# Kernel tuning notes

Measured on AMD Instinct MI355X. Metric: run time of the kernel, lower is better.

Reference implementation:

```python
import jax, jax.numpy as jnp
import numpy as np
from jax import lax

B, NR, NT, M, NUM_ITER = 16384, 64, 32, 4, 64


def setup_inputs() -> dict:
    key = jax.random.key(0)
    k1, k2, k3 = jax.random.split(key, 3)
    yt = jax.random.normal(k1, (B, NR), dtype=jnp.float32)
    # scale channel to keep the 64-step unrolled descent numerically stable
    Ht = 0.1 * jax.random.normal(k2, (B, NR, NT), dtype=jnp.float32)
    sigmat0 = 0.5 + 0.5 * jax.random.uniform(k3, (B,), dtype=jnp.float32)
    m = jnp.array([-3.0, -1.0, 1.0, 3.0], dtype=jnp.float32)          # 4-PAM constellation
    alpha = jnp.full((M,), 0.25, dtype=jnp.float32)                    # uniform prior
    taui = jnp.ones((NUM_ITER + 1,), dtype=jnp.float32)                # taui0 = 1
    delta = jnp.full((NUM_ITER,), 0.1, dtype=jnp.float32)              # delta0 = 0.1
    return {"yt": yt, "Ht": Ht, "sigmat0": sigmat0, "m": m, "alpha": alpha,
            "taui": taui, "delta": delta}


def reference(yt, Ht, sigmat0, m, alpha, taui, delta):
    # Precompute as in CMDNet.call
    HH = jnp.einsum('bri,brj->bij', Ht, Ht)          # [B, Nt, Nt] = H^T H
    yH = jnp.einsum('br,brj->bj', yt, Ht)            # [B, Nt]     = y^T H
    Bsz, _, Nt = Ht.shape
    Mc = m.shape[0]
    n_iter = delta.shape[0]

    G0 = jnp.zeros((Bsz, Nt, Mc), dtype=Ht.dtype)
    sig2 = (sigmat0 ** 2)[:, None, None]             # [B,1,1]
    log_alpha = jnp.log(alpha)                       # [M]
    taui_abs = jnp.abs(taui)                         # [num_iter+1]
    # first layer uses scale 1 in the softmax (first_iter=True), but taui_abs in grad_x
    ft_scale = taui_abs[:n_iter].at[0].set(1.0)

    def step(G, inp):
        scale, ta, d = inp
        ft = jax.nn.softmax((log_alpha + G) * scale, axis=-1)   # [B,Nt,M]
        xt = jnp.sum(ft * m, axis=-1)                           # [B,Nt] soft symbol
        xHH = jnp.einsum('bi,bij->bj', xt, HH)                  # [B,Nt]
        grad_x = ta * (ft * m - ft * xt[..., None])             # [B,Nt,M]
        grad_L = sig2 * (1.0 - jnp.exp(-G)) + grad_x * (xHH - yH)[..., None]
        return G - d * grad_L, None

    G, _ = lax.scan(step, G0, (ft_scale, taui_abs[:n_iter], delta))

    # last layer (last_iter=True): softmax + soft symbol only, no update
    ft = jax.nn.softmax((log_alpha + G) * taui_abs[n_iter], axis=-1)
    xt = jnp.sum(ft * m, axis=-1)
    return ft, xt
```

## Files before the change

### kernel.cpp

```cpp
#include <hip/hip_runtime.h>


#define NRr 64
#define NTt 32
#define NITER 64
#define B_TOTAL 16384

using f16x8  = __attribute__((ext_vector_type(8))) _Float16;
using f32x16 = __attribute__((ext_vector_type(16))) float;

__global__ __launch_bounds__(256) void cmdnet_kernel(
    const float* __restrict__ yt,
    const float* __restrict__ Ht,
    const float* __restrict__ sig0,
    const float* __restrict__ mm,
    const float* __restrict__ alpha,
    const float* __restrict__ taui,
    const float* __restrict__ delta,
    float* __restrict__ out)
{
    __shared__ float xts[4][2][32];

    const int tid = threadIdx.x;
    const int w   = tid >> 6;
    const int l   = tid & 63;
    const int j   = l & 31;
    const int hi  = l >> 5;
    const int b0  = (blockIdx.x * 4 + w) * 2;

    f32x16 accA = {}, accB = {};
    float  ypA = 0.f, ypB = 0.f;
#pragma unroll
    for (int bb = 0; bb < 2; ++bb) {
        const int b = b0 + bb;
        const float* hp = Ht + (size_t)b * NRr * NTt + j;
        const float* yp = yt + (size_t)b * NRr;
        f32x16 acc = {};
        float  ypart = 0.f;
#pragma unroll
        for (int kc = 0; kc < 4; ++kc) {
            const int kb = kc * 16 + hi * 8;
            float h[8];
#pragma unroll
            for (int e = 0; e < 8; ++e) h[e] = hp[(size_t)(kb + e) * NTt];
            const float4 ya = *(const float4*)(yp + kb);
            const float4 yb = *(const float4*)(yp + kb + 4);
            ypart += h[0]*ya.x + h[1]*ya.y + h[2]*ya.z + h[3]*ya.w
                   + h[4]*yb.x + h[5]*yb.y + h[6]*yb.z + h[7]*yb.w;
            f16x8 fa;
#pragma unroll
            for (int e = 0; e < 8; ++e) fa[e] = (_Float16)h[e];
            acc = __builtin_amdgcn_mfma_f32_32x32x16_f16(fa, fa, acc, 0, 0, 0);
        }
        if (bb == 0) { accA = acc; ypA = ypart; }
        else         { accB = acc; ypB = ypart; }
    }

    float hh[32];
#pragma unroll
    for (int r = 0; r < 16; ++r) {
        const float own = hi ? accB[r] : accA[r];
        const float snd = hi ? accA[r] : accB[r];
        const float oth = __shfl_xor(snd, 32, 64);
        const int g = r >> 2, k = r & 3;
        hh[8*g + k]     = hi ? oth : own;
        hh[8*g + 4 + k] = hi ? own : oth;
    }
    const float yA = ypA + __shfl_xor(ypA, 32, 64);
    const float yB = ypB + __shfl_xor(ypB, 32, 64);
    const float yH = hi ? yB : yA;

    const int   bmy  = b0 + hi;
    const float sgv  = sig0[bmy];
    const float sig2 = sgv * sgv;

    const float4 mv = *(const float4*)mm;
    const float4 av = *(const float4*)alpha;
    const float m0 = mv.x, m1 = mv.y, m2 = mv.z, m3 = mv.w;
    const float la0 = __logf(av.x), la1 = __logf(av.y),
                la2 = __logf(av.z), la3 = __logf(av.w);

    float G0 = 0.f, G1 = 0.f, G2 = 0.f, G3 = 0.f;

    for (int it = 0; it < NITER; ++it) {
        const float ta = fabsf(taui[it]);
        const float sc = (it == 0) ? 1.0f : ta;
        const float d  = delta[it];

        const float s0 = (la0 + G0) * sc, s1 = (la1 + G1) * sc;
        const float s2 = (la2 + G2) * sc, s3 = (la3 + G3) * sc;
        const float mx = fmaxf(fmaxf(s0, s1), fmaxf(s2, s3));
        const float e0 = __expf(s0 - mx), e1 = __expf(s1 - mx);
        const float e2 = __expf(s2 - mx), e3 = __expf(s3 - mx);
        const float Z  = (e0 + e1) + (e2 + e3);
        const float R  = __builtin_amdgcn_rcpf(Z);
        const float ft0 = e0 * R, ft1 = e1 * R, ft2 = e2 * R, ft3 = e3 * R;
        const float xt  = (ft0*m0 + ft1*m1) + (ft2*m2 + ft3*m3);

        xts[w][hi][j] = xt;
        asm volatile("" ::: "memory");
        float acc = 0.f;
        const float4* xv = (const float4*)&xts[w][hi][0];
#pragma unroll
        for (int q = 0; q < 8; ++q) {
            const float4 x4 = xv[q];
            acc += hh[4*q+0]*x4.x + hh[4*q+1]*x4.y
                 + hh[4*q+2]*x4.z + hh[4*q+3]*x4.w;
        }
        asm volatile("" ::: "memory");

        const float qd  = acc - yH;
        const float tqd = ta * qd * d;
        const float ds2 = d * sig2;
        G0 -= ds2 * (1.f - __expf(-G0)) + tqd * (ft0 * (m0 - xt));
        G1 -= ds2 * (1.f - __expf(-G1)) + tqd * (ft1 * (m1 - xt));
        G2 -= ds2 * (1.f - __expf(-G2)) + tqd * (ft2 * (m2 - xt));
        G3 -= ds2 * (1.f - __expf(-G3)) + tqd * (ft3 * (m3 - xt));
    }

    {
        const float ta = fabsf(taui[NITER]);
        const float s0 = (la0 + G0) * ta, s1 = (la1 + G1) * ta;
        const float s2 = (la2 + G2) * ta, s3 = (la3 + G3) * ta;
        const float mx = fmaxf(fmaxf(s0, s1), fmaxf(s2, s3));
        const float e0 = __expf(s0 - mx), e1 = __expf(s1 - mx);
        const float e2 = __expf(s2 - mx), e3 = __expf(s3 - mx);
        const float Z  = (e0 + e1) + (e2 + e3);
        const float R  = __builtin_amdgcn_rcpf(Z);
        const float ft0 = e0 * R, ft1 = e1 * R, ft2 = e2 * R, ft3 = e3 * R;
        const float xt  = (ft0*m0 + ft1*m1) + (ft2*m2 + ft3*m3);

        float4 f4; f4.x = ft0; f4.y = ft1; f4.z = ft2; f4.w = ft3;
        *(float4*)(out + ((size_t)bmy * NTt + j) * 4) = f4;
        out[(size_t)B_TOTAL * NTt * 4 + (size_t)bmy * NTt + j] = xt;
    }
}

extern "C" void kernel_launch(void* const* d_in, const int* in_sizes, int n_in,
                              void* d_out, int out_size, void* d_ws, size_t ws_size,
                              hipStream_t stream) {
    const float* yt    = (const float*)d_in[0];
    const float* Ht    = (const float*)d_in[1];
    const float* sig0  = (const float*)d_in[2];
    const float* mm    = (const float*)d_in[3];
    const float* alpha = (const float*)d_in[4];
    const float* taui  = (const float*)d_in[5];
    const float* delta = (const float*)d_in[6];
    float* out = (float*)d_out;

    const int blocks = B_TOTAL / 8;
    cmdnet_kernel<<<blocks, 256, 0, stream>>>(yt, Ht, sig0, mm, alpha, taui,
                                              delta, out);
}
```

Baseline: 115.3 us.

## Pack Gram matrix and soft symbols to fp16 and use dot2 in iteration loop

Stores the per-thread row of H^T H as packed fp16 pairs and writes soft symbols to shared memory in fp16. The mat-vec then runs on v_dot2 instructions with two accumulators, halving LDS reads and register use for hh. The change also swaps exp for exp2 with pre-scaled log2e constants, folds the softmax normalisation into a single scale, and adds an occupancy hint to launch_bounds. The risk is reduced precision: fp16 rounding of the Gram matrix and of xt compounds over 64 iterations.

After: 120.6 us. 1.05x slower.

```diff
diff --git a/kernel.cpp b/kernel.cpp
--- a/kernel.cpp
+++ b/kernel.cpp
@@ -7,9 +7,34 @@
 #define B_TOTAL 16384
 
 using f16x8  = __attribute__((ext_vector_type(8))) _Float16;
+using h16x2  = __attribute__((ext_vector_type(2))) _Float16;
 using f32x16 = __attribute__((ext_vector_type(16))) float;
 
-__global__ __launch_bounds__(256) void cmdnet_kernel(
+static __device__ __forceinline__ uint32_t pk16(float a, float b) {
+    union { _Float16 h[2]; uint32_t u; } x;
+    x.h[0] = (_Float16)a; x.h[1] = (_Float16)b;
+    return x.u;
+}
+
+static __device__ __forceinline__ float fdot2u(uint32_t a, uint32_t b, float c) {
+    union { uint32_t u; h16x2 h; } x, y;
+    x.u = a; y.u = b;
+#if __has_builtin(__builtin_amdgcn_fdot2)
+    return __builtin_amdgcn_fdot2(x.h, y.h, c, false);
+#else
+    return c + (float)x.h[0] * (float)y.h[0] + (float)x.h[1] * (float)y.h[1];
+#endif
+}
+
+static __device__ __forceinline__ float exp2fast(float x) {
+#if __has_builtin(__builtin_amdgcn_exp2f)
+    return __builtin_amdgcn_exp2f(x);
+#else
+    return exp2f(x);
+#endif
+}
+
+__global__ __launch_bounds__(256, 8) void cmdnet_kernel(
     const float* __restrict__ yt,
     const float* __restrict__ Ht,
     const float* __restrict__ sig0,
@@ -19,7 +44,7 @@
     const float* __restrict__ delta,
     float* __restrict__ out)
 {
-    __shared__ float xts[4][2][32];
+    __shared__ __align__(16) _Float16 xtsh[4][2][32];
 
     const int tid = threadIdx.x;
     const int w   = tid >> 6;
@@ -28,8 +53,8 @@
     const int hi  = l >> 5;
     const int b0  = (blockIdx.x * 4 + w) * 2;
 
-    f32x16 accA = {}, accB = {};
-    float  ypA = 0.f, ypB = 0.f;
+    uint32_t apA[8], apB[8];
+    float    ypA = 0.f, ypB = 0.f;
 #pragma unroll
     for (int bb = 0; bb < 2; ++bb) {
         const int b = b0 + bb;
@@ -52,19 +77,32 @@
             for (int e = 0; e < 8; ++e) fa[e] = (_Float16)h[e];
             acc = __builtin_amdgcn_mfma_f32_32x32x16_f16(fa, fa, acc, 0, 0, 0);
         }
-        if (bb == 0) { accA = acc; ypA = ypart; }
-        else         { accB = acc; ypB = ypart; }
-    }
-
-    float hh[32];
-#pragma unroll
-    for (int r = 0; r < 16; ++r) {
-        const float own = hi ? accB[r] : accA[r];
-        const float snd = hi ? accA[r] : accB[r];
-        const float oth = __shfl_xor(snd, 32, 64);
-        const int g = r >> 2, k = r & 3;
-        hh[8*g + k]     = hi ? oth : own;
-        hh[8*g + 4 + k] = hi ? own : oth;
+        uint32_t ap[8];
+#pragma unroll
+        for (int g = 0; g < 4; ++g) {
+            ap[2*g+0] = pk16(acc[4*g+0], acc[4*g+1]);
+            ap[2*g+1] = pk16(acc[4*g+2], acc[4*g+3]);
+        }
+        if (bb == 0) {
+#pragma unroll
+            for (int p = 0; p < 8; ++p) apA[p] = ap[p];
+            ypA = ypart;
+        } else {
+#pragma unroll
+            for (int p = 0; p < 8; ++p) apB[p] = ap[p];
+            ypB = ypart;
+        }
+    }
+
+    uint32_t hh2[16];
+#pragma unroll
+    for (int p = 0; p < 8; ++p) {
+        const uint32_t snd = hi ? apA[p] : apB[p];
+        const uint32_t rcv = (uint32_t)__shfl_xor((int)snd, 32, 64);
+        const uint32_t own = hi ? apB[p] : apA[p];
+        const int g = p >> 1, c = p & 1;
+        hh2[4*g + c]     = hi ? rcv : own;
+        hh2[4*g + 2 + c] = hi ? own : rcv;
     }
     const float yA = ypA + __shfl_xor(ypA, 32, 64);
     const float yB = ypB + __shfl_xor(ypB, 32, 64);
@@ -80,55 +118,67 @@
     const float la0 = __logf(av.x), la1 = __logf(av.y),
                 la2 = __logf(av.z), la3 = __logf(av.w);
 
+    const float L2E  = 1.4426950408889634f;
+    const float NL2E = -1.4426950408889634f;
+
+    _Float16*    xwp = &xtsh[w][hi][j];
+    const uint4* xrp = (const uint4*)&xtsh[w][hi][0];
+
     float G0 = 0.f, G1 = 0.f, G2 = 0.f, G3 = 0.f;
 
     for (int it = 0; it < NITER; ++it) {
-        const float ta = fabsf(taui[it]);
-        const float sc = (it == 0) ? 1.0f : ta;
-        const float d  = delta[it];
-
-        const float s0 = (la0 + G0) * sc, s1 = (la1 + G1) * sc;
-        const float s2 = (la2 + G2) * sc, s3 = (la3 + G3) * sc;
+        const float ta  = fabsf(taui[it]);
+        const float sc2 = ((it == 0) ? 1.0f : ta) * L2E;
+        const float d   = delta[it];
+
+        const float s0 = (la0 + G0) * sc2, s1 = (la1 + G1) * sc2;
+        const float s2 = (la2 + G2) * sc2, s3 = (la3 + G3) * sc2;
         const float mx = fmaxf(fmaxf(s0, s1), fmaxf(s2, s3));
-        const float e0 = __expf(s0 - mx), e1 = __expf(s1 - mx);
-        const float e2 = __expf(s2 - mx), e3 = __expf(s3 - mx);
+        const float e0 = exp2fast(s0 - mx), e1 = exp2fast(s1 - mx);
+        const float e2 = exp2fast(s2 - mx), e3 = exp2fast(s3 - mx);
+        const float Z  = (e0 + e1) + (e2 + e3);
+        const float R  = __builtin_amdgcn_rcpf(Z);
+        const float S  = fmaf(e0, m0, fmaf(e1, m1, fmaf(e2, m2, e3 * m3)));
+        const float xt = S * R;
+
+        *xwp = (_Float16)xt;
+        asm volatile("" ::: "memory");
+        const uint4 xa = xrp[0], xb = xrp[1], xc = xrp[2], xd = xrp[3];
+
+        const float en0 = exp2fast(G0 * NL2E), en1 = exp2fast(G1 * NL2E);
+        const float en2 = exp2fast(G2 * NL2E), en3 = exp2fast(G3 * NL2E);
+
+        float A0 = 0.f, A1 = 0.f;
+        A0 = fdot2u(hh2[ 0], xa.x, A0); A1 = fdot2u(hh2[ 1], xa.y, A1);
+        A0 = fdot2u(hh2[ 2], xa.z, A0); A1 = fdot2u(hh2[ 3], xa.w, A1);
+        A0 = fdot2u(hh2[ 4], xb.x, A0); A1 = fdot2u(hh2[ 5], xb.y, A1);
+        A0 = fdot2u(hh2[ 6], xb.z, A0); A1 = fdot2u(hh2[ 7], xb.w, A1);
+        A0 = fdot2u(hh2[ 8], xc.x, A0); A1 = fdot2u(hh2[ 9], xc.y, A1);
+        A0 = fdot2u(hh2[10], xc.z, A0); A1 = fdot2u(hh2[11], xc.w, A1);
+        A0 = fdot2u(hh2[12], xd.x, A0); A1 = fdot2u(hh2[13], xd.y, A1);
+        A0 = fdot2u(hh2[14], xd.z, A0); A1 = fdot2u(hh2[15], xd.w, A1);
+
+        const float qd   = (A0 + A1) - yH;
+        const float tqdR = (ta * d) * qd * R;
+        const float c1   = d * sig2;
+
+        G0 = fmaf(-tqdR, e0 * (m0 - xt), fmaf(c1, en0, G0 - c1));
+        G1 = fmaf(-tqdR, e1 * (m1 - xt), fmaf(c1, en1, G1 - c1));
+        G2 = fmaf(-tqdR, e2 * (m2 - xt), fmaf(c1, en2, G2 - c1));
+        G3 = fmaf(-tqdR, e3 * (m3 - xt), fmaf(c1, en3, G3 - c1));
+    }
+
+    {
+        const float ta = fabsf(taui[NITER]) * L2E;
+        const float s0 = (la0 + G0) * ta, s1 = (la1 + G1) * ta;
+        const float s2 = (la2 + G2) * ta, s3 = (la3 + G3) * ta;
+        const float mx = fmaxf(fmaxf(s0, s1), fmaxf(s2, s3));
+        const float e0 = exp2fast(s0 - mx), e1 = exp2fast(s1 - mx);
+        const float e2 = exp2fast(s2 - mx), e3 = exp2fast(s3 - mx);
         const float Z  = (e0 + e1) + (e2 + e3);
         const float R  = __builtin_amdgcn_rcpf(Z);
         const float ft0 = e0 * R, ft1 = e1 * R, ft2 = e2 * R, ft3 = e3 * R;
-        const float xt  = (ft0*m0 + ft1*m1) + (ft2*m2 + ft3*m3);
-
-        xts[w][hi][j] = xt;
-        asm volatile("" ::: "memory");
-        float acc = 0.f;
-        const float4* xv = (const float4*)&xts[w][hi][0];
-#pragma unroll
-        for (int q = 0; q < 8; ++q) {
-            const float4 x4 = xv[q];
-            acc += hh[4*q+0]*x4.x + hh[4*q+1]*x4.y
-                 + hh[4*q+2]*x4.z + hh[4*q+3]*x4.w;
-        }
-        asm volatile("" ::: "memory");
-
-        const float qd  = acc - yH;
-        const float tqd = ta * qd * d;
-        const float ds2 = d * sig2;
-        G0 -= ds2 * (1.f - __expf(-G0)) + tqd * (ft0 * (m0 - xt));
-        G1 -= ds2 * (1.f - __expf(-G1)) + tqd * (ft1 * (m1 - xt));
-        G2 -= ds2 * (1.f - __expf(-G2)) + tqd * (ft2 * (m2 - xt));
-        G3 -= ds2 * (1.f - __expf(-G3)) + tqd * (ft3 * (m3 - xt));
-    }
-
-    {
-        const float ta = fabsf(taui[NITER]);
-        const float s0 = (la0 + G0) * ta, s1 = (la1 + G1) * ta;
-        const float s2 = (la2 + G2) * ta, s3 = (la3 + G3) * ta;
-        const float mx = fmaxf(fmaxf(s0, s1), fmaxf(s2, s3));
-        const float e0 = __expf(s0 - mx), e1 = __expf(s1 - mx);
-        const float e2 = __expf(s2 - mx), e3 = __expf(s3 - mx);
-        const float Z  = (e0 + e1) + (e2 + e3);
-        const float R  = __builtin_amdgcn_rcpf(Z);
-        const float ft0 = e0 * R, ft1 = e1 * R, ft2 = e2 * R, ft3 = e3 * R;
-        const float xt  = (ft0*m0 + ft1*m1) + (ft2*m2 + ft3*m3);
+        const float xt  = fmaf(ft0, m0, fmaf(ft1, m1, fmaf(ft2, m2, ft3 * m3)));
 
         float4 f4; f4.x = ft0; f4.y = ft1; f4.z = ft2; f4.w = ft3;
         *(float4*)(out + ((size_t)bmy * NTt + j) * 4) = f4;
```
